# Performance work log

Measured on AMD Instinct MI355X. Metric: run time of the kernel, lower is better.

The kernel has to match this reference:

```python
import jax, jax.numpy as jnp
import numpy as np

N = 100000      # nodes
E = 800000      # edges
F_IN = 128      # input feature dim
HID = 32        # GAT out_channels per head
H = 4           # heads
HC = HID * H    # 128, concat width (== F_IN by design)
EDIM = 16       # raw edge feature dim
G = 256         # number of graphs in batch
OUT = 2         # output classes
SLOPE = 0.2     # GATConv LeakyReLU negative slope
BN_EPS = 1e-5


def setup_inputs() -> dict:
    key = jax.random.key(0)
    ks = jax.random.split(key, 16)
    s = 0.05
    x = jax.random.normal(ks[0], (N, F_IN), jnp.float32)
    edge_index = jax.random.randint(ks[1], (2, E), 0, N, dtype=jnp.int64)
    edge_attr = jax.random.normal(ks[2], (E, EDIM), jnp.float32)
    batch = jnp.sort(jax.random.randint(ks[3], (N,), 0, G, dtype=jnp.int64))
    edge_fc_W = jax.random.normal(ks[4], (EDIM, HID), jnp.float32) * s
    edge_fc_b = jnp.zeros((HID,), jnp.float32)
    # all 3 GAT layers have in_dim 128 -> H*C 128, so stack them
    Ws = jax.random.normal(ks[5], (3, F_IN, HC), jnp.float32) * s
    att_src = jax.random.normal(ks[6], (3, H, HID), jnp.float32) * s
    att_dst = jax.random.normal(ks[7], (3, H, HID), jnp.float32) * s
    att_edge = jax.random.normal(ks[8], (3, H, HID), jnp.float32) * s
    lin_e = jax.random.normal(ks[9], (3, HID, HC), jnp.float32) * s
    biases = jnp.zeros((3, HC), jnp.float32)
    bn_gamma = jnp.ones((3, HC), jnp.float32)
    bn_beta = jnp.zeros((3, HC), jnp.float32)
    fc_W = jax.random.normal(ks[10], (HC, OUT), jnp.float32) * s
    fc_b = jnp.zeros((OUT,), jnp.float32)
    return {"x": x, "edge_index": edge_index, "edge_attr": edge_attr, "batch": batch,
            "edge_fc_W": edge_fc_W, "edge_fc_b": edge_fc_b, "Ws": Ws,
            "att_src": att_src, "att_dst": att_dst, "att_edge": att_edge,
            "lin_e": lin_e, "biases": biases, "bn_gamma": bn_gamma,
            "bn_beta": bn_beta, "fc_W": fc_W, "fc_b": fc_b}


def _gat_layer(h, e_h, src, dst, W, a_s, a_d, a_e, We, b):
    xl = (h @ W).reshape(N, H, HID)            # [N,H,C]
    el = (e_h @ We).reshape(E, H, HID)         # [E,H,C]
    alpha = ((xl * a_s).sum(-1)[src]           # alpha_src gathered at source
             + (xl * a_d).sum(-1)[dst]         # alpha_dst gathered at target
             + (el * a_e).sum(-1))             # [E,H]
    alpha = jax.nn.leaky_relu(alpha, SLOPE)
    # segment softmax over incoming edges of each destination node
    amax = jax.ops.segment_max(alpha, dst, num_segments=N)
    ealpha = jnp.exp(alpha - amax[dst])
    denom = jax.ops.segment_sum(ealpha, dst, num_segments=N)
    alpha = ealpha / (denom[dst] + 1e-16)
    # weighted scatter-aggregate of source messages
    out = jax.ops.segment_sum(alpha[:, :, None] * xl[src], dst, num_segments=N)
    return out.reshape(N, HC) + b


def reference(x, edge_index, edge_attr, batch, edge_fc_W, edge_fc_b, Ws,
              att_src, att_dst, att_edge, lin_e, biases, bn_gamma, bn_beta,
              fc_W, fc_b):
    src, dst = edge_index[0], edge_index[1]
    e_h = edge_attr @ edge_fc_W + edge_fc_b   # [E, HID]
    h = x
    for l in range(3):
        h = _gat_layer(h, e_h, src, dst, Ws[l], att_src[l], att_dst[l],
                       att_edge[l], lin_e[l], biases[l])
        # BatchNorm1d over node dim (training-mode batch statistics)
        mu = h.mean(0)
        var = h.var(0)
        h = (h - mu) * jax.lax.rsqrt(var + BN_EPS) * bn_gamma[l] + bn_beta[l]
        h = jax.nn.relu(h)
        # dropout_rate = 0.0 -> identity
    # global mean pool per graph
    sums = jax.ops.segment_sum(h, batch, num_segments=G)
    cnt = jax.ops.segment_sum(jnp.ones((N,), h.dtype), batch, num_segments=G)
    pooled = sums / jnp.maximum(cnt, 1.0)[:, None]   # [G, HC]
    return pooled @ fc_W + fc_b                      # [G, OUT]
```

## Files before the change

### kernel.cpp

```cpp
#include <hip/hip_runtime.h>

#define Nn 100000
#define Ee 800000
#define HC 128
#define HID 32
#define NHD 4
#define EDIM 16
#define Gg 256
#define NOUT 2
#define SLOPE 0.2f
#define BN_EPS 1e-5f
#define SCHUNK 1024
#define NSB 98
#define NBAG 6250

typedef unsigned int u32;
typedef unsigned short u16;
typedef short v8s __attribute__((ext_vector_type(8)));
typedef float v4f __attribute__((ext_vector_type(4)));

union PkAB { u32 u[4]; v8s v; };

__device__ __forceinline__ float bflo(u32 u){ return __uint_as_float(u << 16); }
__device__ __forceinline__ float bfhi(u32 u){ return __uint_as_float(u & 0xFFFF0000u); }

__device__ __forceinline__ u32 bf16rne(float x)
{
  u32 b = __float_as_uint(x);
  return (b + 0x7FFFu + ((b >> 16) & 1u)) >> 16;
}
__device__ __forceinline__ u32 packsplit(float x)
{
  u32 hb = bf16rne(x);
  float hf = __uint_as_float(hb << 16);
  u32 lb = bf16rne(x - hf);
  return hb | (lb << 16);
}
__device__ __forceinline__ void split2(float f, u32& hb, u32& lb)
{
  hb = bf16rne(f);
  lb = bf16rne(f - __uint_as_float(hb << 16));
}

__device__ __forceinline__ int lbound(const int* __restrict__ a, int n, int key)
{
  int lo = 0, hi = n;
  while (lo < hi) {
    int mid = (lo + hi) >> 1;
    if (a[mid] < key) lo = mid + 1; else hi = mid;
  }
  return lo;
}

__global__ void compute_K(const float* __restrict__ efcW, const float* __restrict__ efcb,
                          const float* __restrict__ linE, const float* __restrict__ attE,
                          float* __restrict__ Kmat, float* __restrict__ kb,
                          const int* __restrict__ batch, int* __restrict__ gb)
{
  __shared__ float Msh[384];
  int t = threadIdx.x;
  if (t <= Gg) gb[t] = lbound(batch, Nn, t);
  if (t < 384) {
    int l = t >> 7, j = (t >> 2) & 31, h = t & 3;
    float m = 0.f;
    for (int c = 0; c < 32; ++c)
      m += linE[(l*32 + j)*128 + h*32 + c] * attE[(l*4 + h)*32 + c];
    Msh[l*128 + j*4 + h] = m;
  }
  __syncthreads();
  if (t < 192) {
    int k = t / 12, col = t % 12, l = col >> 2, h = col & 3;
    float acc = 0.f;
    for (int j = 0; j < 32; ++j)
      acc += efcW[k*32 + j] * Msh[l*128 + j*4 + h];
    Kmat[k*12 + col] = acc;
  } else if (t < 204) {
    int col = t - 192, l = col >> 2, h = col & 3;
    float acc = 0.f;
    for (int j = 0; j < 32; ++j)
      acc += efcb[j] * Msh[l*128 + j*4 + h];
    kb[col] = acc;
  }
}

__global__ void w_split(const float* __restrict__ Wall, u32* __restrict__ Wf)
{
  int tid = blockIdx.x * 256 + threadIdx.x;
  if (tid >= 3*HC*HC) return;
  int l = tid / (HC*HC);
  int rem = tid - l*HC*HC;
  int k = rem >> 7, n = rem & 127;
  u32 p = packsplit(Wall[tid]);
  int nt = n >> 4, col = n & 15;
  int ks = k >> 5, kin = k & 31, q = kin >> 3, j = kin & 7;
  int half = j >> 2, j4 = j & 3;
  int idx = ((((l*8 + nt)*4 + ks)*2 + half)*64 + q*16 + col)*4 + j4;
  Wf[idx] = p;
}

__global__ void k_hist(const int* __restrict__ dst, int* __restrict__ deg)
{
  int e = blockIdx.x * 256 + threadIdx.x;
  if (e < Ee) atomicAdd(&deg[dst[e]], 1);
}

__global__ void k_bsum(const int* __restrict__ deg, int* __restrict__ bsum)
{
  __shared__ int sh[256];
  int b = blockIdx.x, t = threadIdx.x;
  int s = 0;
  for (int i = t; i < SCHUNK; i += 256) {
    int idx = b*SCHUNK + i;
    if (idx < Nn) s += deg[idx];
  }
  sh[t] = s; __syncthreads();
  for (int o = 128; o; o >>= 1) { if (t < o) sh[t] += sh[t+o]; __syncthreads(); }
  if (!t) bsum[b] = sh[0];
}

__global__ void k_mid(const int* __restrict__ bsum, int* __restrict__ bpre, int* __restrict__ rowp)
{
  __shared__ int sh[NSB];
  int t = threadIdx.x;
  if (t < NSB) sh[t] = bsum[t];
  __syncthreads();
  if (!t) {
    int run = 0;
    for (int i = 0; i < NSB; ++i) { int v = sh[i]; sh[i] = run; run += v; }
    rowp[Nn] = run;
  }
  __syncthreads();
  if (t < NSB) bpre[t] = sh[t];
}

__global__ void k_scan(const int* __restrict__ deg, const int* __restrict__ bpre, int* __restrict__ rowp)
{
  __shared__ int sh[SCHUNK];
  int b = blockIdx.x, t = threadIdx.x;
  for (int i = t; i < SCHUNK; i += 256) {
    int idx = b*SCHUNK + i;
    sh[i] = (idx < Nn) ? deg[idx] : 0;
  }
  __syncthreads();
  if (!t) {
    int run = 0;
    for (int i = 0; i < SCHUNK; ++i) { int v = sh[i]; sh[i] = run; run += v; }
  }
  __syncthreads();
  int base = bpre[b];
  for (int i = t; i < SCHUNK; i += 256) {
    int idx = b*SCHUNK + i;
    if (idx < Nn) rowp[idx] = sh[i] + base;
  }
}

__global__ void k_mkperm(const int* __restrict__ src, const int* __restrict__ dst,
                         const int* __restrict__ rowp, int* __restrict__ fill,
                         uint2* __restrict__ eord)
{
  int e = blockIdx.x * 256 + threadIdx.x;
  if (e >= Ee) return;
  int d = dst[e];
  int pos = rowp[d] + atomicAdd(&fill[d], 1);
  eord[pos] = make_uint2((u32)e, (u32)src[e]);
}

__global__ __launch_bounds__(256) void k_fillpre2(const uint2* __restrict__ eord,
                           const float* __restrict__ eattr,
                           const float* __restrict__ Kmat, const float* __restrict__ kb,
                           u32* __restrict__ recS, uint2* __restrict__ recE)
{
  int t = threadIdx.x;
  int qg = t >> 2, r = t & 3;
  int pos = blockIdx.x * 64 + qg;
  if (pos >= Ee) return;
  uint2 es = eord[pos];
  int e = (int)es.x;
  float4 ea = *(const float4*)(eattr + (size_t)e * EDIM + r*4);
  float part[12];
  #pragma unroll
  for (int col = 0; col < 12; ++col) {
    part[col] = ea.x * Kmat[(r*4+0)*12 + col]
              + ea.y * Kmat[(r*4+1)*12 + col]
              + ea.z * Kmat[(r*4+2)*12 + col]
              + ea.w * Kmat[(r*4+3)*12 + col];
  }
  #pragma unroll
  for (int col = 0; col < 12; ++col) {
    part[col] += __shfl_xor(part[col], 1);
    part[col] += __shfl_xor(part[col], 2);
    part[col] += kb[col];
  }
  if (r < 3) {
    uint2 w;
    w.x = bf16rne(part[4*r+0]) | (bf16rne(part[4*r+1]) << 16);
    w.y = bf16rne(part[4*r+2]) | (bf16rne(part[4*r+3]) << 16);
    recE[(size_t)r*Ee + pos] = w;
  } else {
    recS[pos] = es.y;
  }
}

__global__ __launch_bounds__(256, 4) void gemm_mfma(const u32* __restrict__ Apk,
                                                    const u32* __restrict__ Wf,
                                                    u16* __restrict__ C2,
                                                    const float* __restrict__ aS,
                                                    const float* __restrict__ aD,
                                                    float* __restrict__ as_,
                                                    float* __restrict__ ad_,
                                                    const float* __restrict__ scb,
                                                    const float* __restrict__ shb,
                                                    int mode)
{
  __shared__ uint4 Bsh[1024];
  int t = threadIdx.x;
  int w = t >> 6, lane = t & 63;
  int col = lane & 15, q = lane >> 4;
  int rbase = blockIdx.x * 64 + w * 16;

  v4f acc[8];
  #pragma unroll
  for (int nt = 0; nt < 8; ++nt) acc[nt] = (v4f){0.f, 0.f, 0.f, 0.f};

  const uint4* Wf4 = (const uint4*)Wf;

  int ar = rbase + col;
  if (ar >= Nn) ar = Nn - 1;
  const uint4* pa = (const uint4*)(Apk + (size_t)ar*HC);
  uint4 ra[8];
  #pragma unroll
  for (int ks = 0; ks < 4; ++ks) {
    ra[2*ks]   = pa[ks*8 + q*2];
    ra[2*ks+1] = pa[ks*8 + q*2 + 1];
  }

  for (int ks = 0; ks < 4; ++ks) {
    #pragma unroll
    for (int i = 0; i < 4; ++i) {
      int u = t + i*256;
      int nt = u >> 7, rem = u & 127;
      Bsh[u] = Wf4[((nt*4 + ks)*2 + (rem >> 6))*64 + (rem & 63)];
    }
    __syncthreads();

    PkAB Ah, Al;
    int cb = ks*32 + q*8;
    uint4 r0 = ra[2*ks], r1 = ra[2*ks+1];
    float f0, f1, f2, f3, f4, f5, f6, f7;
    if (mode == 0) {
      f0 = __uint_as_float(r0.x); f1 = __uint_as_float(r0.y);
      f2 = __uint_as_float(r0.z); f3 = __uint_as_float(r0.w);
      f4 = __uint_as_float(r1.x); f5 = __uint_as_float(r1.y);
      f6 = __uint_as_float(r1.z); f7 = __uint_as_float(r1.w);
    } else {
      float4 sc0 = *(const float4*)(scb + cb), sc1 = *(const float4*)(scb + cb + 4);
      float4 sh0 = *(const float4*)(shb + cb), sh1 = *(const float4*)(shb + cb + 4);
      f0 = fmaxf((bflo(r0.x)+bfhi(r0.x))*sc0.x + sh0.x, 0.f);
      f1 = fmaxf((bflo(r0.y)+bfhi(r0.y))*sc0.y + sh0.y, 0.f);
      f2 = fmaxf((bflo(r0.z)+bfhi(r0.z))*sc0.z + sh0.z, 0.f);
      f3 = fmaxf((bflo(r0.w)+bfhi(r0.w))*sc0.w + sh0.w, 0.f);
      f4 = fmaxf((bflo(r1.x)+bfhi(r1.x))*sc1.x + sh1.x, 0.f);
      f5 = fmaxf((bflo(r1.y)+bfhi(r1.y))*sc1.y + sh1.y, 0.f);
      f6 = fmaxf((bflo(r1.z)+bfhi(r1.z))*sc1.z + sh1.z, 0.f);
      f7 = fmaxf((bflo(r1.w)+bfhi(r1.w))*sc1.w + sh1.w, 0.f);
    }
    {
      u32 hb0,lb0,hb1,lb1,hb2,lb2,hb3,lb3,hb4,lb4,hb5,lb5,hb6,lb6,hb7,lb7;
      split2(f0,hb0,lb0); split2(f1,hb1,lb1); split2(f2,hb2,lb2); split2(f3,hb3,lb3);
      split2(f4,hb4,lb4); split2(f5,hb5,lb5); split2(f6,hb6,lb6); split2(f7,hb7,lb7);
      Ah.u[0] = hb0 | (hb1 << 16);  Al.u[0] = lb0 | (lb1 << 16);
      Ah.u[1] = hb2 | (hb3 << 16);  Al.u[1] = lb2 | (lb3 << 16);
      Ah.u[2] = hb4 | (hb5 << 16);  Al.u[2] = lb4 | (lb5 << 16);
      Ah.u[3] = hb6 | (hb7 << 16);  Al.u[3] = lb6 | (lb7 << 16);
    }
    #pragma unroll
    for (int nt = 0; nt < 8; ++nt) {
      uint4 b0 = Bsh[nt*128 + lane];
      uint4 b1 = Bsh[nt*128 + 64 + lane];
      PkAB Bh, Bl;
      Bh.u[0] = (b0.x & 0xFFFFu) | (b0.y << 16);
      Bl.u[0] = (b0.x >> 16)     | (b0.y & 0xFFFF0000u);
      Bh.u[1] = (b0.z & 0xFFFFu) | (b0.w << 16);
      Bl.u[1] = (b0.z >> 16)     | (b0.w & 0xFFFF0000u);
      Bh.u[2] = (b1.x & 0xFFFFu) | (b1.y << 16);
      Bl.u[2] = (b1.x >> 16)     | (b1.y & 0xFFFF0000u);
      Bh.u[3] = (b1.z & 0xFFFFu) | (b1.w << 16);
      Bl.u[3] = (b1.z >> 16)     | (b1.w & 0xFFFF0000u);
      acc[nt] = __builtin_amdgcn_mfma_f32_16x16x32_bf16(Ah.v, Bh.v, acc[nt], 0, 0, 0);
      acc[nt] = __builtin_amdgcn_mfma_f32_16x16x32_bf16(Ah.v, Bl.v, acc[nt], 0, 0, 0);
      acc[nt] = __builtin_amdgcn_mfma_f32_16x16x32_bf16(Al.v, Bh.v, acc[nt], 0, 0, 0);
    }
    __syncthreads();
  }

  #pragma unroll
  for (int reg = 0; reg < 4; ++reg) {
    int row = rbase + q*4 + reg;
    if (row < Nn) {
      #pragma unroll
      for (int nt = 0; nt < 8; ++nt)
        C2[(size_t)row*HC + nt*16 + col] = (u16)bf16rne(acc[nt][reg]);
    }
  }

  #pragma unroll
  for (int h = 0; h < 4; ++h) {
    float a0 = aS[32*h + col], a1 = aS[32*h + 16 + col];
    float d0 = aD[32*h + col], d1 = aD[32*h + 16 + col];
    #pragma unroll
    for (int reg = 0; reg < 4; ++reg) {
      float s1 = acc[2*h][reg]*a0 + acc[2*h+1][reg]*a1;
      float s2 = acc[2*h][reg]*d0 + acc[2*h+1][reg]*d1;
      s1 += __shfl_xor(s1, 1); s1 += __shfl_xor(s1, 2);
      s1 += __shfl_xor(s1, 4); s1 += __shfl_xor(s1, 8);
      s2 += __shfl_xor(s2, 1); s2 += __shfl_xor(s2, 2);
      s2 += __shfl_xor(s2, 4); s2 += __shfl_xor(s2, 8);
      if (col == 0) {
        int row = rbase + q*4 + reg;
        if (row < Nn) {
          as_[row*NHD + h] = s1;
          ad_[row*NHD + h] = s2;
        }
      }
    }
  }
}

__global__ __launch_bounds__(256) void aggregate(const int* __restrict__ rowp,
                                                 const u32* __restrict__ recS,
                                                 const u32* __restrict__ recE,
                                                 const float* __restrict__ as_, const float* __restrict__ ad_,
                                                 int l, const u32* __restrict__ xl2,
                                                 const float* __restrict__ bias, u32* __restrict__ outp,
                                                 float* __restrict__ psum, float* __restrict__ psq)
{
  __shared__ float4 rsA[256], rsB[256], rqA[256], rqB[256];
  int t = threadIdx.x;
  int n = blockIdx.x * 16 + (t >> 4);
  int c8 = t & 15;
  int h = c8 >> 2;
  float o[8];
  #pragma unroll
  for (int k = 0; k < 8; ++k) o[k] = 0.f;
  if (n < Nn) {
    const u32* recEl = recE + (size_t)l * ((size_t)Ee * 2);
    int ph = h >> 1, sel = h & 1;
    float adh = ad_[n*NHD + h];
    int beg = rowp[n], end = rowp[n+1];
    float acc[8];
    #pragma unroll
    for (int k = 0; k < 8; ++k) acc[k] = 0.f;
    float wsum = 0.f;
    int i = beg;
    for (; i + 8 <= end; i += 8) {
      u32 eu[8]; int s[8]; float av[8]; uint4 v[8];
      #pragma unroll
      for (int j = 0; j < 8; ++j) eu[j] = recEl[(size_t)(i+j)*2 + ph];
      #pragma unroll
      for (int j = 0; j < 8; ++j) s[j] = (int)recS[i+j];
      #pragma unroll
      for (int j = 0; j < 8; ++j) av[j] = as_[s[j]*NHD + h];
      #pragma unroll
      for (int j = 0; j < 8; ++j) v[j] = *(const uint4*)(xl2 + (size_t)s[j] * 64 + c8*4);
      #pragma unroll
      for (int j = 0; j < 8; ++j) {
        float ep = sel ? bfhi(eu[j]) : bflo(eu[j]);
        float a = ep + av[j] + adh;
        a = (a > 0.f) ? a : SLOPE * a;
        float wj = __expf(a);
        acc[0] += wj*bflo(v[j].x); acc[1] += wj*bfhi(v[j].x);
        acc[2] += wj*bflo(v[j].y); acc[3] += wj*bfhi(v[j].y);
        acc[4] += wj*bflo(v[j].z); acc[5] += wj*bfhi(v[j].z);
        acc[6] += wj*bflo(v[j].w); acc[7] += wj*bfhi(v[j].w);
        wsum += wj;
      }
    }
    for (; i + 4 <= end; i += 4) {
      u32 eu[4]; int s[4]; float av[4]; uint4 v[4];
      #pragma unroll
      for (int j = 0; j < 4; ++j) eu[j] = recEl[(size_t)(i+j)*2 + ph];
      #pragma unroll
      for (int j = 0; j < 4; ++j) s[j] = (int)recS[i+j];
      #pragma unroll
      for (int j = 0; j < 4; ++j) av[j] = as_[s[j]*NHD + h];
      #pragma unroll
      for (int j = 0; j < 4; ++j) v[j] = *(const uint4*)(xl2 + (size_t)s[j] * 64 + c8*4);
      #pragma unroll
      for (int j = 0; j < 4; ++j) {
        float ep = sel ? bfhi(eu[j]) : bflo(eu[j]);
        float a = ep + av[j] + adh;
        a = (a > 0.f) ? a : SLOPE * a;
        float wj = __expf(a);
        acc[0] += wj*bflo(v[j].x); acc[1] += wj*bfhi(v[j].x);
        acc[2] += wj*bflo(v[j].y); acc[3] += wj*bfhi(v[j].y);
        acc[4] += wj*bflo(v[j].z); acc[5] += wj*bfhi(v[j].z);
        acc[6] += wj*bflo(v[j].w); acc[7] += wj*bfhi(v[j].w);
        wsum += wj;
      }
    }
    for (; i < end; ++i) {
      u32 eu = recEl[(size_t)i*2 + ph];
      int s = (int)recS[i];
      float ep = sel ? bfhi(eu) : bflo(eu);
      float a = ep + as_[s*NHD + h] + adh;
      a = (a > 0.f) ? a : SLOPE * a;
      float wj = __expf(a);
      uint4 v = *(const uint4*)(xl2 + (size_t)s * 64 + c8*4);
      acc[0] += wj*bflo(v.x); acc[1] += wj*bfhi(v.x);
      acc[2] += wj*bflo(v.y); acc[3] += wj*bfhi(v.y);
      acc[4] += wj*bflo(v.z); acc[5] += wj*bfhi(v.z);
      acc[6] += wj*bflo(v.w); acc[7] += wj*bfhi(v.w);
      wsum += wj;
    }
    float inv = 1.f / (wsum + 1e-16f);
    uint4 w0, w1;
    #pragma unroll
    for (int k = 0; k < 8; ++k) o[k] = acc[k]*inv + bias[c8*8 + k];
    w0.x = packsplit(o[0]); w0.y = packsplit(o[1]);
    w0.z = packsplit(o[2]); w0.w = packsplit(o[3]);
    w1.x = packsplit(o[4]); w1.y = packsplit(o[5]);
    w1.z = packsplit(o[6]); w1.w = packsplit(o[7]);
    uint4* op = (uint4*)(outp + (size_t)n * HC + c8*8);
    op[0] = w0; op[1] = w1;
  }
  rsA[t] = make_float4(o[0], o[1], o[2], o[3]);
  rsB[t] = make_float4(o[4], o[5], o[6], o[7]);
  rqA[t] = make_float4(o[0]*o[0], o[1]*o[1], o[2]*o[2], o[3]*o[3]);
  rqB[t] = make_float4(o[4]*o[4], o[5]*o[5], o[6]*o[6], o[7]*o[7]);
  __syncthreads();
  for (int off = 128; off >= 16; off >>= 1) {
    if (t < off) {
      rsA[t].x += rsA[t+off].x; rsA[t].y += rsA[t+off].y;
      rsA[t].z += rsA[t+off].z; rsA[t].w += rsA[t+off].w;
      rsB[t].x += rsB[t+off].x; rsB[t].y += rsB[t+off].y;
      rsB[t].z += rsB[t+off].z; rsB[t].w += rsB[t+off].w;
      rqA[t].x += rqA[t+off].x; rqA[t].y += rqA[t+off].y;
      rqA[t].z += rqA[t+off].z; rqA[t].w += rqA[t+off].w;
      rqB[t].x += rqB[t+off].x; rqB[t].y += rqB[t+off].y;
      rqB[t].z += rqB[t+off].z; rqB[t].w += rqB[t+off].w;
    }
    __syncthreads();
  }
  if (t < 16) {
    float4* ps = (float4*)(psum + (size_t)blockIdx.x*HC + t*8);
    ps[0] = rsA[t]; ps[1] = rsB[t];
    float4* pq = (float4*)(psq + (size_t)blockIdx.x*HC + t*8);
    pq[0] = rqA[t]; pq[1] = rqB[t];
  }
}

__global__ __launch_bounds__(256) void k_bnpartfin(const float* __restrict__ psum, const float* __restrict__ psq,
                                                   float* __restrict__ gsum, float* __restrict__ gsq,
                                                   int* __restrict__ bnctr,
                                                   const float* __restrict__ gammaL, const float* __restrict__ betaL,
                                                   float* __restrict__ scb, float* __restrict__ shb)
{
  __shared__ float4 rs[256], rq[256];
  __shared__ int lastv;
  int t = threadIdx.x;
  int c4 = t & 31, rg = t >> 5;
  float4 s = make_float4(0.f,0.f,0.f,0.f), q = make_float4(0.f,0.f,0.f,0.f);
  for (int k = blockIdx.x*8 + rg; k < NBAG; k += 64*8) {
    float4 a = *(const float4*)(psum + (size_t)k*HC + c4*4);
    float4 b = *(const float4*)(psq  + (size_t)k*HC + c4*4);
    s.x += a.x; s.y += a.y; s.z += a.z; s.w += a.w;
    q.x += b.x; q.y += b.y; q.z += b.z; q.w += b.w;
  }
  rs[t] = s; rq[t] = q;
  __syncthreads();
  for (int off = 128; off >= 32; off >>= 1) {
    if (t < off) {
      rs[t].x += rs[t+off].x; rs[t].y += rs[t+off].y;
      rs[t].z += rs[t+off].z; rs[t].w += rs[t+off].w;
      rq[t].x += rq[t+off].x; rq[t].y += rq[t+off].y;
      rq[t].z += rq[t+off].z; rq[t].w += rq[t+off].w;
    }
    __syncthreads();
  }
  if (t < 32) {
    atomicAdd(&gsum[t*4+0], rs[t].x); atomicAdd(&gsum[t*4+1], rs[t].y);
    atomicAdd(&gsum[t*4+2], rs[t].z); atomicAdd(&gsum[t*4+3], rs[t].w);
    atomicAdd(&gsq[t*4+0], rq[t].x);  atomicAdd(&gsq[t*4+1], rq[t].y);
    atomicAdd(&gsq[t*4+2], rq[t].z);  atomicAdd(&gsq[t*4+3], rq[t].w);
  }
  __syncthreads();
  if (t == 0) {
    __threadfence();
    lastv = (atomicAdd(bnctr, 1) == 63);
  }
  __syncthreads();
  if (lastv) {
    if (t < HC) {
      float sv = atomicAdd(&gsum[t], 0.f);
      float qv = atomicAdd(&gsq[t], 0.f);
      float mu  = sv * (1.f / Nn);
      float var = qv * (1.f / Nn) - mu * mu;
      float sc = rsqrtf(var + BN_EPS) * gammaL[t];
      scb[t] = sc;
      shb[t] = betaL[t] - mu * sc;
      atomicExch(&gsum[t], 0.f);
      atomicExch(&gsq[t], 0.f);
    }
    if (t == 0) atomicExch(bnctr, 0);
  }
}

__global__ __launch_bounds__(256) void pool2(const u32* __restrict__ Ap, const int* __restrict__ gb,
                                             const float* __restrict__ scb, const float* __restrict__ shb,
                                             float* __restrict__ pool)
{
  __shared__ float4 red[256];
  int g = blockIdx.x >> 2, qt = blockIdx.x & 3;
  int t = threadIdx.x;
  int cg = t & 7;
  int rs = t >> 3;
  int c4 = qt*8 + cg;
  int c = c4 * 4;
  int lo = gb[g], hi = gb[g+1];
  float4 s4 = *(const float4*)(scb + c);
  float4 t4 = *(const float4*)(shb + c);
  float4 acc = make_float4(0.f,0.f,0.f,0.f);
  for (int n = lo + rs; n < hi; n += 32) {
    uint4 v = *(const uint4*)(Ap + (size_t)n*HC + c);
    acc.x += fmaxf((bflo(v.x)+bfhi(v.x))*s4.x + t4.x, 0.f);
    acc.y += fmaxf((bflo(v.y)+bfhi(v.y))*s4.y + t4.y, 0.f);
    acc.z += fmaxf((bflo(v.z)+bfhi(v.z))*s4.z + t4.z, 0.f);
    acc.w += fmaxf((bflo(v.w)+bfhi(v.w))*s4.w + t4.w, 0.f);
  }
  red[t] = acc;
  __syncthreads();
  for (int off = 128; off >= 8; off >>= 1) {
    if (t < off) {
      red[t].x += red[t+off].x; red[t].y += red[t+off].y;
      red[t].z += red[t+off].z; red[t].w += red[t+off].w;
    }
    __syncthreads();
  }
  if (t < 8) {
    float inv = 1.f / fmaxf((float)(hi - lo), 1.f);
    float4 r = red[t];
    r.x *= inv; r.y *= inv; r.z *= inv; r.w *= inv;
    *(float4*)(pool + (size_t)g*HC + qt*32 + t*4) = r;
  }
}

__global__ void final_fc(const float* __restrict__ pool,
                         const float* __restrict__ fcW, const float* __restrict__ fcb,
                         float* __restrict__ out)
{
  int t = blockIdx.x * 256 + threadIdx.x;
  if (t >= Gg * NOUT) return;
  int g = t >> 1, o = t & 1;
  float acc = 0.f;
  for (int k = 0; k < HC; ++k)
    acc += pool[(size_t)g * HC + k] * fcW[k * NOUT + o];
  out[t] = acc + fcb[o];
}

extern "C" void kernel_launch(void* const* d_in, const int* in_sizes, int n_in,
                              void* d_out, int out_size, void* d_ws, size_t ws_size,
                              hipStream_t stream)
{
  const float* x      = (const float*)d_in[0];
  const int*   eidx   = (const int*)d_in[1];
  const float* eattr  = (const float*)d_in[2];
  const int*   batch  = (const int*)d_in[3];
  const float* efcW   = (const float*)d_in[4];
  const float* efcb   = (const float*)d_in[5];
  const float* Wall   = (const float*)d_in[6];
  const float* attS   = (const float*)d_in[7];
  const float* attD   = (const float*)d_in[8];
  const float* attE   = (const float*)d_in[9];
  const float* linE   = (const float*)d_in[10];
  const float* biases = (const float*)d_in[11];
  const float* gamma  = (const float*)d_in[12];
  const float* beta   = (const float*)d_in[13];
  const float* fcW    = (const float*)d_in[14];
  const float* fcb    = (const float*)d_in[15];
  float* out = (float*)d_out;

  const int* src = eidx;
  const int* dst = eidx + Ee;

  float* ws    = (float*)d_ws;
  float* bufA  = ws;
  float* bufB  = bufA + (size_t)Nn*HC;
  float* as_   = bufB + (size_t)Nn*HC;
  float* ad_   = as_ + (size_t)Nn*NHD;
  float* Kmat  = ad_ + (size_t)Nn*NHD;
  float* kb    = Kmat + 192;
  float* scb   = kb + 16;
  float* shb   = scb + 128;
  float* pool  = shb + 128;
  u32*   rec   = (u32*)(pool + (size_t)Gg*HC);
  u32*   recS  = rec;
  u32*   recE  = rec + (size_t)Ee;
  u32*   Wf    = rec + (size_t)Ee*8;
  float* psum  = (float*)(Wf + 3*HC*HC);
  float* psq   = psum + (size_t)NBAG*HC;
  int*   gb    = (int*)(psq + (size_t)NBAG*HC);
  int*   rowp  = gb + (Gg + 3);
  int*   deg   = rowp + (Nn + 1);
  int*   fill  = deg + Nn;
  float* gsum  = (float*)(fill + Nn);
  float* gsq   = gsum + 128;
  int*   bnctr = (int*)(gsq + 128);
  int*   bsum  = bnctr + 4;
  int*   bpre  = bsum + 128;
  uint2* eord  = (uint2*)bufB;

  w_split<<<(3*HC*HC + 255)/256, 256, 0, stream>>>(Wall, Wf);
  compute_K<<<1, 512, 0, stream>>>(efcW, efcb, linE, attE, Kmat, kb, batch, gb);

  hipMemsetAsync(deg, 0, (size_t)(2*Nn + 260) * sizeof(int), stream);
  k_hist<<<(Ee + 255)/256, 256, 0, stream>>>(dst, deg);
  k_bsum<<<NSB, 256, 0, stream>>>(deg, bsum);
  k_mid<<<1, 128, 0, stream>>>(bsum, bpre, rowp);
  k_scan<<<NSB, 256, 0, stream>>>(deg, bpre, rowp);
  k_mkperm<<<(Ee + 255)/256, 256, 0, stream>>>(src, dst, rowp, fill, eord);
  k_fillpre2<<<(Ee + 63)/64, 256, 0, stream>>>(eord, eattr, Kmat, kb, recS, (uint2*)recE);

  for (int l = 0; l < 3; ++l) {
    const u32* A = (l == 0) ? (const u32*)x : (const u32*)bufA;
    gemm_mfma<<<(Nn + 63)/64, 256, 0, stream>>>(A, Wf + (size_t)l*HC*HC, (u16*)bufB,
                                                attS + l*HC, attD + l*HC, as_, ad_,
                                                scb, shb, (l > 0) ? 1 : 0);
    aggregate<<<NBAG, 256, 0, stream>>>(rowp, recS, recE, as_, ad_, l, (const u32*)bufB,
                                        biases + l*HC, (u32*)bufA, psum, psq);
    k_bnpartfin<<<64, 256, 0, stream>>>(psum, psq, gsum, gsq, bnctr,
                                        gamma + l*HC, beta + l*HC, scb, shb);
  }

  pool2<<<Gg*4, 256, 0, stream>>>((const u32*)bufA, gb, scb, shb, pool);
  final_fc<<<2, 256, 0, stream>>>(pool, fcW, fcb, out);
}
```

Baseline: 626.7 us.

## Split each node's edge list across four lane groups in aggregation

The aggregate kernel now gives each destination node a full 64-lane wavefront instead of 16 lanes. Four 16-lane groups each walk a strided subset of the node's incoming edges, and their partial sums are combined with cross-lane shuffles. Blocks grow to 512 threads covering 8 nodes, which doubles the number of blocks and of BatchNorm partial-statistic slots. The goal is more memory-level parallelism for the irregular gathers and shorter per-lane loops at an average degree of 8. The cost is extra shuffle reductions, idle lanes on low-degree nodes, and a larger shared-memory reduction.

```diff
diff --git a/kernel.cpp b/kernel.cpp
--- a/kernel.cpp
+++ b/kernel.cpp
@@ -12,7 +12,8 @@
 #define BN_EPS 1e-5f
 #define SCHUNK 1024
 #define NSB 98
-#define NBAG 6250
+#define NPB 8
+#define NBAG 12500
 
 typedef unsigned int u32;
 typedef unsigned short u16;
@@ -326,7 +327,7 @@
   }
 }
 
-__global__ __launch_bounds__(256) void aggregate(const int* __restrict__ rowp,
+__global__ __launch_bounds__(512) void aggregate(const int* __restrict__ rowp,
                                                  const u32* __restrict__ recS,
                                                  const u32* __restrict__ recE,
                                                  const float* __restrict__ as_, const float* __restrict__ ad_,
@@ -334,10 +335,11 @@
                                                  const float* __restrict__ bias, u32* __restrict__ outp,
                                                  float* __restrict__ psum, float* __restrict__ psq)
 {
-  __shared__ float4 rsA[256], rsB[256], rqA[256], rqB[256];
+  __shared__ float4 rsA[512], rsB[512], rqA[512], rqB[512];
   int t = threadIdx.x;
-  int n = blockIdx.x * 16 + (t >> 4);
+  int n = blockIdx.x * NPB + (t >> 6);
   int c8 = t & 15;
+  int el = (t >> 4) & 3;
   int h = c8 >> 2;
   float o[8];
   #pragma unroll
@@ -351,84 +353,70 @@
     #pragma unroll
     for (int k = 0; k < 8; ++k) acc[k] = 0.f;
     float wsum = 0.f;
-    int i = beg;
-    for (; i + 8 <= end; i += 8) {
-      u32 eu[8]; int s[8]; float av[8]; uint4 v[8];
-      #pragma unroll
-      for (int j = 0; j < 8; ++j) eu[j] = recEl[(size_t)(i+j)*2 + ph];
-      #pragma unroll
-      for (int j = 0; j < 8; ++j) s[j] = (int)recS[i+j];
-      #pragma unroll
-      for (int j = 0; j < 8; ++j) av[j] = as_[s[j]*NHD + h];
-      #pragma unroll
-      for (int j = 0; j < 8; ++j) v[j] = *(const uint4*)(xl2 + (size_t)s[j] * 64 + c8*4);
-      #pragma unroll
-      for (int j = 0; j < 8; ++j) {
-        float ep = sel ? bfhi(eu[j]) : bflo(eu[j]);
-        float a = ep + av[j] + adh;
-        a = (a > 0.f) ? a : SLOPE * a;
-        float wj = __expf(a);
-        acc[0] += wj*bflo(v[j].x); acc[1] += wj*bfhi(v[j].x);
-        acc[2] += wj*bflo(v[j].y); acc[3] += wj*bfhi(v[j].y);
-        acc[4] += wj*bflo(v[j].z); acc[5] += wj*bfhi(v[j].z);
-        acc[6] += wj*bflo(v[j].w); acc[7] += wj*bfhi(v[j].w);
-        wsum += wj;
-      }
-    }
-    for (; i + 4 <= end; i += 4) {
-      u32 eu[4]; int s[4]; float av[4]; uint4 v[4];
-      #pragma unroll
-      for (int j = 0; j < 4; ++j) eu[j] = recEl[(size_t)(i+j)*2 + ph];
-      #pragma unroll
-      for (int j = 0; j < 4; ++j) s[j] = (int)recS[i+j];
-      #pragma unroll
-      for (int j = 0; j < 4; ++j) av[j] = as_[s[j]*NHD + h];
-      #pragma unroll
-      for (int j = 0; j < 4; ++j) v[j] = *(const uint4*)(xl2 + (size_t)s[j] * 64 + c8*4);
-      #pragma unroll
-      for (int j = 0; j < 4; ++j) {
-        float ep = sel ? bfhi(eu[j]) : bflo(eu[j]);
-        float a = ep + av[j] + adh;
-        a = (a > 0.f) ? a : SLOPE * a;
-        float wj = __expf(a);
-        acc[0] += wj*bflo(v[j].x); acc[1] += wj*bfhi(v[j].x);
-        acc[2] += wj*bflo(v[j].y); acc[3] += wj*bfhi(v[j].y);
-        acc[4] += wj*bflo(v[j].z); acc[5] += wj*bfhi(v[j].z);
-        acc[6] += wj*bflo(v[j].w); acc[7] += wj*bfhi(v[j].w);
-        wsum += wj;
-      }
-    }
-    for (; i < end; ++i) {
+    int i = beg + el;
+    for (; i + 4 < end; i += 8) {
+      u32 eu0 = recEl[(size_t)i*2 + ph];
+      u32 eu1 = recEl[(size_t)(i+4)*2 + ph];
+      int s0 = (int)recS[i], s1 = (int)recS[i+4];
+      float av0 = as_[s0*NHD + h], av1 = as_[s1*NHD + h];
+      uint4 v0 = *(const uint4*)(xl2 + (size_t)s0 * 64 + c8*4);
+      uint4 v1 = *(const uint4*)(xl2 + (size_t)s1 * 64 + c8*4);
+      float a0 = (sel ? bfhi(eu0) : bflo(eu0)) + av0 + adh;
+      a0 = (a0 > 0.f) ? a0 : SLOPE * a0;
+      float w0 = __expf(a0);
+      float a1 = (sel ? bfhi(eu1) : bflo(eu1)) + av1 + adh;
+      a1 = (a1 > 0.f) ? a1 : SLOPE * a1;
+      float w1 = __expf(a1);
+      acc[0] += w0*bflo(v0.x); acc[1] += w0*bfhi(v0.x);
+      acc[2] += w0*bflo(v0.y); acc[3] += w0*bfhi(v0.y);
+      acc[4] += w0*bflo(v0.z); acc[5] += w0*bfhi(v0.z);
+      acc[6] += w0*bflo(v0.w); acc[7] += w0*bfhi(v0.w);
+      acc[0] += w1*bflo(v1.x); acc[1] += w1*bfhi(v1.x);
+      acc[2] += w1*bflo(v1.y); acc[3] += w1*bfhi(v1.y);
+      acc[4] += w1*bflo(v1.z); acc[5] += w1*bfhi(v1.z);
+      acc[6] += w1*bflo(v1.w); acc[7] += w1*bfhi(v1.w);
+      wsum += w0 + w1;
+    }
+    if (i < end) {
       u32 eu = recEl[(size_t)i*2 + ph];
       int s = (int)recS[i];
-      float ep = sel ? bfhi(eu) : bflo(eu);
-      float a = ep + as_[s*NHD + h] + adh;
+      float av = as_[s*NHD + h];
+      uint4 v = *(const uint4*)(xl2 + (size_t)s * 64 + c8*4);
+      float a = (sel ? bfhi(eu) : bflo(eu)) + av + adh;
       a = (a > 0.f) ? a : SLOPE * a;
       float wj = __expf(a);
-      uint4 v = *(const uint4*)(xl2 + (size_t)s * 64 + c8*4);
       acc[0] += wj*bflo(v.x); acc[1] += wj*bfhi(v.x);
       acc[2] += wj*bflo(v.y); acc[3] += wj*bfhi(v.y);
       acc[4] += wj*bflo(v.z); acc[5] += wj*bfhi(v.z);
       acc[6] += wj*bflo(v.w); acc[7] += wj*bfhi(v.w);
       wsum += wj;
     }
-    float inv = 1.f / (wsum + 1e-16f);
-    uint4 w0, w1;
     #pragma unroll
-    for (int k = 0; k < 8; ++k) o[k] = acc[k]*inv + bias[c8*8 + k];
-    w0.x = packsplit(o[0]); w0.y = packsplit(o[1]);
-    w0.z = packsplit(o[2]); w0.w = packsplit(o[3]);
-    w1.x = packsplit(o[4]); w1.y = packsplit(o[5]);
-    w1.z = packsplit(o[6]); w1.w = packsplit(o[7]);
-    uint4* op = (uint4*)(outp + (size_t)n * HC + c8*8);
-    op[0] = w0; op[1] = w1;
+    for (int k = 0; k < 8; ++k) {
+      acc[k] += __shfl_xor(acc[k], 16);
+      acc[k] += __shfl_xor(acc[k], 32);
+    }
+    wsum += __shfl_xor(wsum, 16);
+    wsum += __shfl_xor(wsum, 32);
+    if (el == 0) {
+      float inv = 1.f / (wsum + 1e-16f);
+      uint4 w0, w1;
+      #pragma unroll
+      for (int k = 0; k < 8; ++k) o[k] = acc[k]*inv + bias[c8*8 + k];
+      w0.x = packsplit(o[0]); w0.y = packsplit(o[1]);
+      w0.z = packsplit(o[2]); w0.w = packsplit(o[3]);
+      w1.x = packsplit(o[4]); w1.y = packsplit(o[5]);
+      w1.z = packsplit(o[6]); w1.w = packsplit(o[7]);
+      uint4* op = (uint4*)(outp + (size_t)n * HC + c8*8);
+      op[0] = w0; op[1] = w1;
+    }
   }
   rsA[t] = make_float4(o[0], o[1], o[2], o[3]);
   rsB[t] = make_float4(o[4], o[5], o[6], o[7]);
   rqA[t] = make_float4(o[0]*o[0], o[1]*o[1], o[2]*o[2], o[3]*o[3]);
   rqB[t] = make_float4(o[4]*o[4], o[5]*o[5], o[6]*o[6], o[7]*o[7]);
   __syncthreads();
-  for (int off = 128; off >= 16; off >>= 1) {
+  for (int off = 256; off >= 16; off >>= 1) {
     if (t < off) {
       rsA[t].x += rsA[t+off].x; rsA[t].y += rsA[t+off].y;
       rsA[t].z += rsA[t+off].z; rsA[t].w += rsA[t+off].w;
@@ -625,7 +613,7 @@
     gemm_mfma<<<(Nn + 63)/64, 256, 0, stream>>>(A, Wf + (size_t)l*HC*HC, (u16*)bufB,
                                                 attS + l*HC, attD + l*HC, as_, ad_,
                                                 scb, shb, (l > 0) ? 1 : 0);
-    aggregate<<<NBAG, 256, 0, stream>>>(rowp, recS, recE, as_, ad_, l, (const u32*)bufB,
+    aggregate<<<NBAG, 512, 0, stream>>>(rowp, recS, recE, as_, ad_, l, (const u32*)bufB,
                                         biases + l*HC, (u32*)bufA, psum, psq);
     k_bnpartfin<<<64, 256, 0, stream>>>(psum, psq, gsum, gsq, bnctr,
                                         gamma + l*HC, beta + l*HC, scb, shb);
```

After: 651.3 us. +3.9%, slower.
